# Kernel optimization log

Hardware: AMD Instinct MI355X
Metric: run time of the kernel (lower is better)

## Reference

```python
import jax, jax.numpy as jnp
import numpy as np

H = W = 32
C = 384
NH = 12
HEAD = C // NH
SCALE = HEAD ** -0.5
WS = 8            # window size
SS = 4            # shift size
N = WS * WS       # tokens per window (64)
NW = (H // WS) * (W // WS)  # windows per image (16)
HIDDEN = 4 * C
EPS = 1e-5
SQRT_2_OVER_PI = float(np.sqrt(2.0 / np.pi))


def _relative_position_index():
    ch = np.arange(WS)
    coords = np.stack(np.meshgrid(ch, ch, indexing='ij')).reshape(2, -1)  # [2, N]
    rel = (coords[:, :, None] - coords[:, None, :]).transpose(1, 2, 0)    # [N, N, 2]
    rel[:, :, 0] += WS - 1
    rel[:, :, 1] += WS - 1
    rel[:, :, 0] *= 2 * WS - 1
    return rel.sum(-1)  # [N, N] int


def _attn_mask():
    img = np.zeros((H, W), np.float32)
    sl = (slice(0, -WS), slice(-WS, -SS), slice(-SS, None))
    cnt = 0
    for hs in sl:
        for ws_ in sl:
            img[hs, ws_] = cnt
            cnt += 1
    m = img.reshape(H // WS, WS, W // WS, WS).transpose(0, 2, 1, 3).reshape(-1, N)  # [nW, N]
    am = m[:, None, :] - m[:, :, None]
    return np.where(am != 0, -100.0, 0.0).astype(np.float32)  # [nW, N, N]


REL_IDX = jnp.asarray(_relative_position_index())
ATTN_MASK = jnp.asarray(_attn_mask())


def _gelu(x):
    return x * 0.5 * (1.0 + jnp.tanh(SQRT_2_OVER_PI * (x + 0.044715 * x ** 3)))


def _layernorm(x, g, b):
    mu = jnp.mean(x, axis=-1, keepdims=True)
    var = jnp.mean(jnp.square(x - mu), axis=-1, keepdims=True)
    return (x - mu) * jax.lax.rsqrt(var + EPS) * g + b


def _window_partition(x):  # [B,H,W,C] -> [B*nW, N, C]
    B = x.shape[0]
    x = x.reshape(B, H // WS, WS, W // WS, WS, C).transpose(0, 1, 3, 2, 4, 5)
    return x.reshape(-1, N, C)


def _window_reverse(w, B):  # [B*nW, N, C] -> [B,H,W,C]
    x = w.reshape(B, H // WS, W // WS, WS, WS, C).transpose(0, 1, 3, 2, 4, 5)
    return x.reshape(B, H, W, C)


def setup_inputs() -> dict:
    key = jax.random.key(0)
    ks = jax.random.split(key, 16)
    s = 0.02
    return {
        'x': jax.random.normal(ks[0], (32, H * W, C), jnp.float32),
        'norm1_g': jnp.ones((C,), jnp.float32),
        'norm1_b': jnp.zeros((C,), jnp.float32),
        'qkv_w': jax.random.normal(ks[1], (C, 3 * C), jnp.float32) * s,
        'qkv_b': jnp.zeros((3 * C,), jnp.float32),
        'rel_bias_table': jax.random.normal(ks[2], ((2 * WS - 1) ** 2, NH), jnp.float32) * s,
        'proj_w': jax.random.normal(ks[3], (C, C), jnp.float32) * s,
        'proj_b': jnp.zeros((C,), jnp.float32),
        'norm2_g': jnp.ones((C,), jnp.float32),
        'norm2_b': jnp.zeros((C,), jnp.float32),
        'fc1_w': jax.random.normal(ks[4], (C, HIDDEN), jnp.float32) * s,
        'fc1_b': jnp.zeros((HIDDEN,), jnp.float32),
        'fc2_w': jax.random.normal(ks[5], (HIDDEN, C), jnp.float32) * s,
        'fc2_b': jnp.zeros((C,), jnp.float32),
    }


def reference(x, norm1_g, norm1_b, qkv_w, qkv_b, rel_bias_table, proj_w, proj_b,
              norm2_g, norm2_b, fc1_w, fc1_b, fc2_w, fc2_b):
    B = x.shape[0]
    shortcut = x
    y = _layernorm(x, norm1_g, norm1_b).reshape(B, H, W, C)
    y = jnp.roll(y, shift=(-SS, -SS), axis=(1, 2))          # cyclic shift
    win = _window_partition(y)                               # [B*nW, N, C]

    qkv = (win @ qkv_w + qkv_b).reshape(-1, N, 3, NH, HEAD).transpose(2, 0, 3, 1, 4)
    q, k, v = qkv[0], qkv[1], qkv[2]                         # [B*nW, NH, N, HEAD]
    attn = jnp.einsum('whnd,whmd->whnm', q * SCALE, k)       # [B*nW, NH, N, N]

    bias = rel_bias_table[REL_IDX.reshape(-1)].reshape(N, N, NH).transpose(2, 0, 1)
    attn = attn + bias[None]
    attn = attn.reshape(B, NW, NH, N, N) + ATTN_MASK[None, :, None]
    attn = jax.nn.softmax(attn.reshape(-1, NH, N, N), axis=-1)

    out = jnp.einsum('whnm,whmd->wnhd', attn, v).reshape(-1, N, C)
    out = out @ proj_w + proj_b                              # [B*nW, N, C]

    y = _window_reverse(out, B)
    y = jnp.roll(y, shift=(SS, SS), axis=(1, 2)).reshape(B, H * W, C)

    x = shortcut + y                                         # drop_path is identity (eval)
    h = _layernorm(x, norm2_g, norm2_b)
    h = _gelu(h @ fc1_w + fc1_b) @ fc2_w + fc2_b
    return x + h
```

## Files before the change

kernel.cpp:

```cpp
#include <hip/hip_runtime.h>
#include <hip/hip_bf16.h>
#include <math.h>

typedef __hip_bfloat16 bf16;
typedef __attribute__((ext_vector_type(8))) short short8;
typedef __attribute__((ext_vector_type(4))) float floatx4;

static constexpr int TOK = 32768;
static constexpr int CDIM = 384;
static constexpr int HID = 1536;

__device__ __forceinline__ bf16 f2bf(float v) { return __float2bfloat16(v); }

__device__ __forceinline__ unsigned short bf_bits(float a) {
  bf16 h = __float2bfloat16(a);
  unsigned short u;
  __builtin_memcpy(&u, &h, 2);
  return u;
}
__device__ __forceinline__ unsigned pack2(float a, float b) {
  return (unsigned)bf_bits(a) | ((unsigned)bf_bits(b) << 16);
}

typedef const __attribute__((address_space(1))) unsigned gas_t;
typedef __attribute__((address_space(3))) unsigned las_t;
__device__ __forceinline__ void gload16(const bf16* g, const bf16* l) {
  __builtin_amdgcn_global_load_lds((gas_t*)g, (las_t*)l, 16, 0, 0);
}

__global__ void k_convt(const float* __restrict__ src, bf16* __restrict__ dst,
                        int Kd, int Nd) {
  int tid = blockIdx.x * 256 + threadIdx.x;
  if (tid >= Kd * Nd) return;
  int k = tid / Nd, n = tid - k * Nd;
  dst[(size_t)n * Kd + k] = f2bf(src[tid]);
}

__global__ __launch_bounds__(256) void k_ln1(const float* __restrict__ x,
                                             const float* __restrict__ g,
                                             const float* __restrict__ b,
                                             bf16* __restrict__ out) {
  int wt = blockIdx.x * 4 + (threadIdx.x >> 6);
  int lane = threadIdx.x & 63;
  int win = wt >> 6, ntok = wt & 63;
  int bimg = win >> 4, wi = win & 15;
  int sh = (((wi >> 2) << 3) + (ntok >> 3) + 4) & 31;
  int sw = (((wi & 3) << 3) + (ntok & 7) + 4) & 31;
  const float* xr = x + ((size_t)bimg * 1024 + sh * 32 + sw) * CDIM;
  float v[6]; float s = 0.f, ss = 0.f;
#pragma unroll
  for (int j = 0; j < 6; ++j) {
    float t = xr[j * 64 + lane];
    v[j] = t; s += t; ss += t * t;
  }
#pragma unroll
  for (int off = 32; off > 0; off >>= 1) {
    s += __shfl_xor(s, off, 64);
    ss += __shfl_xor(ss, off, 64);
  }
  float mu = s * (1.f / 384.f);
  float var = ss * (1.f / 384.f) - mu * mu;
  float rs = rsqrtf(var + 1e-5f);
  bf16* orow = out + (size_t)wt * CDIM;
#pragma unroll
  for (int j = 0; j < 6; ++j) {
    int c = j * 64 + lane;
    orow[c] = f2bf((v[j] - mu) * rs * g[c] + b[c]);
  }
}

__global__ __launch_bounds__(256) void k_ln2(const float* __restrict__ x1,
                                             const float* __restrict__ g,
                                             const float* __restrict__ b,
                                             bf16* __restrict__ out) {
  int t = blockIdx.x * 4 + (threadIdx.x >> 6);
  int lane = threadIdx.x & 63;
  const float* xr = x1 + (size_t)t * CDIM;
  float v[6]; float s = 0.f, ss = 0.f;
#pragma unroll
  for (int j = 0; j < 6; ++j) {
    float q = xr[j * 64 + lane];
    v[j] = q; s += q; ss += q * q;
  }
#pragma unroll
  for (int off = 32; off > 0; off >>= 1) {
    s += __shfl_xor(s, off, 64);
    ss += __shfl_xor(ss, off, 64);
  }
  float mu = s * (1.f / 384.f);
  float var = ss * (1.f / 384.f) - mu * mu;
  float rs = rsqrtf(var + 1e-5f);
  bf16* orow = out + (size_t)t * CDIM;
#pragma unroll
  for (int j = 0; j < 6; ++j) {
    int c = j * 64 + lane;
    orow[c] = f2bf((v[j] - mu) * rs * g[c] + b[c]);
  }
}

template <int K, int EPI, int NT>
__global__ __launch_bounds__(256) void k_gemm(const bf16* __restrict__ A,
                                              const bf16* __restrict__ Bt,
                                              const float* __restrict__ bias,
                                              const float* __restrict__ extra,
                                              void* __restrict__ outp) {
  __shared__ __attribute__((aligned(16))) char pool[32768];
  bf16* As = (bf16*)pool;
  bf16* Bs = (bf16*)(pool + 16384);

  const int tid = threadIdx.x;
  const int wv = tid >> 6, lane = tid & 63;

  const int flat = blockIdx.x;
  const int xcd = flat & 7;
  const int idx = flat >> 3;
  const int rpx = (gridDim.x >> 3) / NT;
  const int cb = idx % NT;
  const int rb = idx / NT;
  const int mblk = (xcd * rpx + rb) * 128, nblk = cb * 128;

  const int srow = lane >> 3;
  const int scol8 = (lane & 7) ^ srow;
  const bf16* gaw = A + (size_t)(mblk + wv * 32 + srow) * K + scol8 * 8;
  const bf16* gbw = Bt + (size_t)(nblk + wv * 32 + srow) * K + scol8 * 8;
  const bf16* lAw = As + wv * 2048;
  const bf16* lBw = Bs + wv * 2048;

  const int wr = wv >> 1, wc = wv & 1;
  const int mr = lane & 15, q = lane >> 4;
  const bf16* faRow = As + (wr * 64 + mr) * 64;
  const bf16* fbRow = Bs + (wc * 64 + mr) * 64;
  const int sw0 = (q ^ (mr & 7)) * 8;
  const int sw4 = ((q + 4) ^ (mr & 7)) * 8;

  floatx4 acc[4][4];
#pragma unroll
  for (int i = 0; i < 4; ++i)
#pragma unroll
    for (int j = 0; j < 4; ++j) acc[i][j] = floatx4{0.f, 0.f, 0.f, 0.f};

  for (int k0 = 0; k0 < K; k0 += 64) {
    __syncthreads();
#pragma unroll
    for (int c = 0; c < 4; ++c) gload16(gaw + k0 + c * 8 * K, lAw + c * 512);
#pragma unroll
    for (int c = 0; c < 4; ++c) gload16(gbw + k0 + c * 8 * K, lBw + c * 512);
    __syncthreads();
    {
      short8 a[4], b[4];
#pragma unroll
      for (int mt = 0; mt < 4; ++mt) a[mt] = *(const short8*)(faRow + mt * 1024 + sw0);
#pragma unroll
      for (int nt = 0; nt < 4; ++nt) b[nt] = *(const short8*)(fbRow + nt * 1024 + sw0);
#pragma unroll
      for (int mt = 0; mt < 4; ++mt)
#pragma unroll
        for (int nt = 0; nt < 4; ++nt)
          acc[mt][nt] = __builtin_amdgcn_mfma_f32_16x16x32_bf16(a[mt], b[nt], acc[mt][nt], 0, 0, 0);
    }
    {
      short8 a[4], b[4];
#pragma unroll
      for (int mt = 0; mt < 4; ++mt) a[mt] = *(const short8*)(faRow + mt * 1024 + sw4);
#pragma unroll
      for (int nt = 0; nt < 4; ++nt) b[nt] = *(const short8*)(fbRow + nt * 1024 + sw4);
#pragma unroll
      for (int mt = 0; mt < 4; ++mt)
#pragma unroll
        for (int nt = 0; nt < 4; ++nt)
          acc[mt][nt] = __builtin_amdgcn_mfma_f32_16x16x32_bf16(a[mt], b[nt], acc[mt][nt], 0, 0, 0);
    }
  }

  __syncthreads();
  float* epsw = (float*)pool + wv * (16 * 68);
  const int rr = lane >> 2, c0 = (lane & 3) * 16;
#pragma unroll
  for (int mt = 0; mt < 4; ++mt) {
#pragma unroll
    for (int nt = 0; nt < 4; ++nt)
#pragma unroll
      for (int r = 0; r < 4; ++r)
        epsw[(q * 4 + r) * 68 + nt * 16 + mr] = acc[mt][nt][r];
    float v[16];
#pragma unroll
    for (int j = 0; j < 4; ++j) {
      float4 t = *(const float4*)&epsw[rr * 68 + c0 + j * 4];
      v[j * 4 + 0] = t.x; v[j * 4 + 1] = t.y; v[j * 4 + 2] = t.z; v[j * 4 + 3] = t.w;
    }
    const int grow = mblk + wr * 64 + mt * 16 + rr;
    const int gcol = nblk + wc * 64 + c0;

    if constexpr (EPI == 0) {
      int win = grow >> 6, ntok = grow & 63;
      int s = gcol / 384;
      int rem = gcol - s * 384;
      int h = rem >> 5, d0 = rem & 31;
      bf16* op = (bf16*)outp + (((size_t)s * 512 + win) * 12 + h) * 2048 + ntok * 32 + d0;
      uint4 pk;
      float bv[16];
#pragma unroll
      for (int j = 0; j < 16; ++j) bv[j] = v[j] + bias[gcol + j];
      pk.x = pack2(bv[0], bv[1]); pk.y = pack2(bv[2], bv[3]);
      pk.z = pack2(bv[4], bv[5]); pk.w = pack2(bv[6], bv[7]);
      *(uint4*)op = pk;
      pk.x = pack2(bv[8], bv[9]); pk.y = pack2(bv[10], bv[11]);
      pk.z = pack2(bv[12], bv[13]); pk.w = pack2(bv[14], bv[15]);
      *(uint4*)(op + 8) = pk;
    } else if constexpr (EPI == 1) {
      int win = grow >> 6, ntok = grow & 63;
      int bimg = win >> 4, wi = win & 15;
      int hh = (((wi >> 2) << 3) + (ntok >> 3) + 4) & 31;
      int ww = (((wi & 3) << 3) + (ntok & 7) + 4) & 31;
      size_t t = (size_t)bimg * 1024 + hh * 32 + ww;
      float* op = (float*)outp + t * CDIM + gcol;
      const float* xr = extra + t * CDIM + gcol;
#pragma unroll
      for (int j = 0; j < 4; ++j) {
        float4 xv = *(const float4*)(xr + j * 4);
        float4 ov;
        ov.x = xv.x + v[j * 4 + 0] + bias[gcol + j * 4 + 0];
        ov.y = xv.y + v[j * 4 + 1] + bias[gcol + j * 4 + 1];
        ov.z = xv.z + v[j * 4 + 2] + bias[gcol + j * 4 + 2];
        ov.w = xv.w + v[j * 4 + 3] + bias[gcol + j * 4 + 3];
        *(float4*)(op + j * 4) = ov;
      }
    } else if constexpr (EPI == 2) {
      float gv[16];
#pragma unroll
      for (int j = 0; j < 16; ++j) {
        float z = v[j] + bias[gcol + j];
        float u = 0.7978845608028654f * (z + 0.044715f * z * z * z);
        gv[j] = z / (1.f + __expf(-2.f * u));
      }
      bf16* op = (bf16*)outp + (size_t)grow * HID + gcol;
      uint4 pk;
      pk.x = pack2(gv[0], gv[1]); pk.y = pack2(gv[2], gv[3]);
      pk.z = pack2(gv[4], gv[5]); pk.w = pack2(gv[6], gv[7]);
      *(uint4*)op = pk;
      pk.x = pack2(gv[8], gv[9]); pk.y = pack2(gv[10], gv[11]);
      pk.z = pack2(gv[12], gv[13]); pk.w = pack2(gv[14], gv[15]);
      *(uint4*)(op + 8) = pk;
    } else {
      float* op = (float*)outp + (size_t)grow * CDIM + gcol;
      const float* xr = extra + (size_t)grow * CDIM + gcol;
#pragma unroll
      for (int j = 0; j < 4; ++j) {
        float4 xv = *(const float4*)(xr + j * 4);
        float4 ov;
        ov.x = xv.x + v[j * 4 + 0] + bias[gcol + j * 4 + 0];
        ov.y = xv.y + v[j * 4 + 1] + bias[gcol + j * 4 + 1];
        ov.z = xv.z + v[j * 4 + 2] + bias[gcol + j * 4 + 2];
        ov.w = xv.w + v[j * 4 + 3] + bias[gcol + j * 4 + 3];
        *(float4*)(op + j * 4) = ov;
      }
    }
  }
}

__global__ __launch_bounds__(64) void k_attn(const bf16* __restrict__ qkv,
                                             const float* __restrict__ tblg,
                                             bf16* __restrict__ out) {
  __shared__ __attribute__((aligned(16))) char pool[16384];
  bf16* Qs = (bf16*)pool;
  bf16* Ks = (bf16*)(pool + 5120);
  bf16* Ps = (bf16*)pool;
  float* Os = (float*)pool;
  bf16* Vt = (bf16*)(pool + 10240);
  unsigned long long* msk = (unsigned long long*)(pool + 14848);
  float* tbl = (float*)(pool + 15360);

  const int bid = blockIdx.x;
  const int win = bid / 12, head = bid - win * 12;
  const int lane = threadIdx.x;
  const int q = lane >> 4, mr = lane & 15;

  for (int i = lane; i < 225; i += 64) tbl[i] = tblg[i * 12 + head];

  size_t base = ((size_t)win * 12 + head) * 2048 + lane * 32;
  const uint4* qp = (const uint4*)(qkv + base);
  const uint4* kp = (const uint4*)(qkv + (size_t)12582912 + base);
  const uint4* vp = (const uint4*)(qkv + (size_t)25165824 + base);
#pragma unroll
  for (int i = 0; i < 4; ++i) *(uint4*)(Qs + lane * 40 + i * 8) = qp[i];
#pragma unroll
  for (int i = 0; i < 4; ++i) *(uint4*)(Ks + lane * 40 + i * 8) = kp[i];
  {
    union { uint4 u[4]; unsigned short h[32]; } vv;
#pragma unroll
    for (int i = 0; i < 4; ++i) vv.u[i] = vp[i];
    unsigned short* VtU = (unsigned short*)Vt;
#pragma unroll
    for (int d = 0; d < 32; ++d) VtU[d * 72 + lane] = vv.h[d];
  }
  {
    int wi = win & 15;
    int ri = lane >> 3, ci = lane & 7;
    int rh = ((wi >> 2) << 3) + ri, rw = ((wi & 3) << 3) + ci;
    int rid = (rh < 24 ? 0 : (rh < 28 ? 1 : 2)) * 3 + (rw < 24 ? 0 : (rw < 28 ? 1 : 2));
    unsigned long long m = 0;
#pragma unroll
    for (int v = 0; v < 9; ++v) {
      unsigned long long bb = __ballot(rid == v);
      if (rid == v) m = bb;
    }
    msk[lane] = m;
  }

  floatx4 sac[4][4];
#pragma unroll
  for (int i = 0; i < 4; ++i)
#pragma unroll
    for (int j = 0; j < 4; ++j) sac[i][j] = floatx4{0.f, 0.f, 0.f, 0.f};
  {
    short8 af[4], bf[4];
#pragma unroll
    for (int t = 0; t < 4; ++t) af[t] = *(const short8*)(Qs + (t * 16 + mr) * 40 + q * 8);
#pragma unroll
    for (int t = 0; t < 4; ++t) bf[t] = *(const short8*)(Ks + (t * 16 + mr) * 40 + q * 8);
#pragma unroll
    for (int mt = 0; mt < 4; ++mt)
#pragma unroll
      for (int nt = 0; nt < 4; ++nt)
        sac[mt][nt] = __builtin_amdgcn_mfma_f32_16x16x32_bf16(af[mt], bf[nt], sac[mt][nt], 0, 0, 0);
  }

  float psum[4][4];
#pragma unroll
  for (int mt = 0; mt < 4; ++mt)
#pragma unroll
    for (int r = 0; r < 4; ++r) psum[mt][r] = 0.f;
#pragma unroll
  for (int mt = 0; mt < 4; ++mt) {
#pragma unroll
    for (int r = 0; r < 4; ++r) {
      const int i = mt * 16 + q * 4 + r;
      const unsigned long long mrow = msk[i];
      const int bi = (i >> 3) * 15 + (i & 7);
#pragma unroll
      for (int nt = 0; nt < 4; ++nt) {
        const int j = nt * 16 + mr;
        const int idx = bi + 112 - (j >> 3) * 15 - (j & 7);
        float val = sac[mt][nt][r] * 0.17677669529663687f + tbl[idx];
        float p = __expf(val);
        p = ((mrow >> j) & 1ull) ? p : 0.f;
        psum[mt][r] += p;
        Ps[i * 72 + j] = f2bf(p);
      }
    }
  }
  float inv[4][4];
#pragma unroll
  for (int mt = 0; mt < 4; ++mt)
#pragma unroll
    for (int r = 0; r < 4; ++r) {
      float s = psum[mt][r];
      s += __shfl_xor(s, 1, 64);
      s += __shfl_xor(s, 2, 64);
      s += __shfl_xor(s, 4, 64);
      s += __shfl_xor(s, 8, 64);
      inv[mt][r] = 1.f / s;
    }

  floatx4 oac[4][2];
#pragma unroll
  for (int i = 0; i < 4; ++i)
#pragma unroll
    for (int j = 0; j < 2; ++j) oac[i][j] = floatx4{0.f, 0.f, 0.f, 0.f};
#pragma unroll
  for (int kk = 0; kk < 2; ++kk) {
    short8 ap[4], bv[2];
#pragma unroll
    for (int mt = 0; mt < 4; ++mt)
      ap[mt] = *(const short8*)(Ps + (mt * 16 + mr) * 72 + kk * 32 + q * 8);
#pragma unroll
    for (int nt = 0; nt < 2; ++nt)
      bv[nt] = *(const short8*)(Vt + (nt * 16 + mr) * 72 + kk * 32 + q * 8);
#pragma unroll
    for (int mt = 0; mt < 4; ++mt)
#pragma unroll
      for (int nt = 0; nt < 2; ++nt)
        oac[mt][nt] = __builtin_amdgcn_mfma_f32_16x16x32_bf16(ap[mt], bv[nt], oac[mt][nt], 0, 0, 0);
  }

#pragma unroll
  for (int mt = 0; mt < 4; ++mt)
#pragma unroll
    for (int nt = 0; nt < 2; ++nt)
#pragma unroll
      for (int r = 0; r < 4; ++r)
        Os[(mt * 16 + q * 4 + r) * 40 + nt * 16 + mr] = oac[mt][nt][r] * inv[mt][r];
  float ov[32];
#pragma unroll
  for (int c = 0; c < 8; ++c) {
    const int cc = c ^ (lane & 7);
    float4 t = *(const float4*)(Os + lane * 40 + cc * 4);
    ov[cc * 4 + 0] = t.x; ov[cc * 4 + 1] = t.y;
    ov[cc * 4 + 2] = t.z; ov[cc * 4 + 3] = t.w;
  }
  uint4* o4 = (uint4*)(out + ((size_t)win * 64 + lane) * CDIM + head * 32);
#pragma unroll
  for (int i = 0; i < 4; ++i) {
    uint4 pk;
    pk.x = pack2(ov[i * 8 + 0], ov[i * 8 + 1]);
    pk.y = pack2(ov[i * 8 + 2], ov[i * 8 + 3]);
    pk.z = pack2(ov[i * 8 + 4], ov[i * 8 + 5]);
    pk.w = pack2(ov[i * 8 + 6], ov[i * 8 + 7]);
    o4[i] = pk;
  }
}

extern "C" void kernel_launch(void* const* d_in, const int* in_sizes, int n_in,
                              void* d_out, int out_size, void* d_ws, size_t ws_size,
                              hipStream_t stream) {
  const float* x = (const float*)d_in[0];
  const float* n1g = (const float*)d_in[1];
  const float* n1b = (const float*)d_in[2];
  const float* qkv_w = (const float*)d_in[3];
  const float* qkv_b = (const float*)d_in[4];
  const float* reltbl = (const float*)d_in[5];
  const float* proj_w = (const float*)d_in[6];
  const float* proj_b = (const float*)d_in[7];
  const float* n2g = (const float*)d_in[8];
  const float* n2b = (const float*)d_in[9];
  const float* fc1_w = (const float*)d_in[10];
  const float* fc1_b = (const float*)d_in[11];
  const float* fc2_w = (const float*)d_in[12];
  const float* fc2_b = (const float*)d_in[13];
  float* out = (float*)d_out;

  char* p = (char*)d_ws;
  bf16* w_qkv_t = (bf16*)p;  p += (size_t)442368 * 2;
  bf16* w_proj_t = (bf16*)p; p += (size_t)147456 * 2;
  bf16* w_fc1_t = (bf16*)p;  p += (size_t)589824 * 2;
  bf16* w_fc2_t = (bf16*)p;  p += (size_t)589824 * 2;
  bf16* bufA = (bf16*)p;     p += (size_t)12582912 * 2;
  bf16* qkvb = (bf16*)p;     p += (size_t)37748736 * 2;
  bf16* attno = (bf16*)p;    p += (size_t)12582912 * 2;
  float* x1 = (float*)p;     p += (size_t)12582912 * 4;
  bf16* hidden = qkvb;

  k_convt<<<dim3((442368 + 255) / 256), dim3(256), 0, stream>>>(qkv_w, w_qkv_t, 384, 1152);
  k_convt<<<dim3((147456 + 255) / 256), dim3(256), 0, stream>>>(proj_w, w_proj_t, 384, 384);
  k_convt<<<dim3((589824 + 255) / 256), dim3(256), 0, stream>>>(fc1_w, w_fc1_t, 384, 1536);
  k_convt<<<dim3((589824 + 255) / 256), dim3(256), 0, stream>>>(fc2_w, w_fc2_t, 1536, 384);

  k_ln1<<<dim3(8192), dim3(256), 0, stream>>>(x, n1g, n1b, bufA);
  k_gemm<384, 0, 9><<<dim3(9 * 256), dim3(256), 0, stream>>>(bufA, w_qkv_t, qkv_b, nullptr, qkvb);
  k_attn<<<dim3(6144), dim3(64), 0, stream>>>(qkvb, reltbl, attno);
  k_gemm<384, 1, 3><<<dim3(3 * 256), dim3(256), 0, stream>>>(attno, w_proj_t, proj_b, x, x1);
  k_ln2<<<dim3(8192), dim3(256), 0, stream>>>(x1, n2g, n2b, bufA);
  k_gemm<384, 2, 12><<<dim3(12 * 256), dim3(256), 0, stream>>>(bufA, w_fc1_t, fc1_b, nullptr, hidden);
  k_gemm<1536, 3, 3><<<dim3(3 * 256), dim3(256), 0, stream>>>(hidden, w_fc2_t, fc2_b, x1, out);
}
```

Before: 435.8 us.

## Register-prefetch GEMM tiles and use narrower N tiles for N=384 GEMMs

Replaces the direct global-to-LDS loads with register-staged prefetch: the next K slice is loaded into registers while MFMAs run on the current LDS tile, then written to LDS at the top of the next iteration. It also adds a TN template parameter so the proj and fc2 GEMMs (N=384) use 128x64 tiles. This doubles their grid from 768 to 1536 blocks for better CU occupancy, at the cost of less reuse of A. The register staging raises VGPR use and loses the async LDS-load path.

```diff
diff --git a/kernel.cpp b/kernel.cpp
--- a/kernel.cpp
+++ b/kernel.cpp
@@ -20,12 +20,6 @@
 }
 __device__ __forceinline__ unsigned pack2(float a, float b) {
   return (unsigned)bf_bits(a) | ((unsigned)bf_bits(b) << 16);
-}
-
-typedef const __attribute__((address_space(1))) unsigned gas_t;
-typedef __attribute__((address_space(3))) unsigned las_t;
-__device__ __forceinline__ void gload16(const bf16* g, const bf16* l) {
-  __builtin_amdgcn_global_load_lds((gas_t*)g, (las_t*)l, 16, 0, 0);
 }
 
 __global__ void k_convt(const float* __restrict__ src, bf16* __restrict__ dst,
@@ -98,13 +92,15 @@
   }
 }
 
-template <int K, int EPI, int NT>
+template <int K, int EPI, int NT, int TN>
 __global__ __launch_bounds__(256) void k_gemm(const bf16* __restrict__ A,
                                               const bf16* __restrict__ Bt,
                                               const float* __restrict__ bias,
                                               const float* __restrict__ extra,
                                               void* __restrict__ outp) {
-  __shared__ __attribute__((aligned(16))) char pool[32768];
+  constexpr int NB = (TN == 128) ? 4 : 2;
+  constexpr int MT = (TN == 128) ? 4 : 2;
+  __shared__ __attribute__((aligned(16))) char pool[16384 + NB * 4096];
   bf16* As = (bf16*)pool;
   bf16* Bs = (bf16*)(pool + 16384);
 
@@ -117,55 +113,68 @@
   const int rpx = (gridDim.x >> 3) / NT;
   const int cb = idx % NT;
   const int rb = idx / NT;
-  const int mblk = (xcd * rpx + rb) * 128, nblk = cb * 128;
+  const int mblk = (xcd * rpx + rb) * 128, nblk = cb * TN;
 
   const int srow = lane >> 3;
   const int scol8 = (lane & 7) ^ srow;
   const bf16* gaw = A + (size_t)(mblk + wv * 32 + srow) * K + scol8 * 8;
-  const bf16* gbw = Bt + (size_t)(nblk + wv * 32 + srow) * K + scol8 * 8;
-  const bf16* lAw = As + wv * 2048;
-  const bf16* lBw = Bs + wv * 2048;
-
-  const int wr = wv >> 1, wc = wv & 1;
+  const bf16* gbw = Bt + (size_t)(nblk + wv * (NB * 8) + srow) * K + scol8 * 8;
+
+  const int wrow = (TN == 128) ? (wv >> 1) * 64 : wv * 32;
+  const int wcol = (TN == 128) ? (wv & 1) * 64 : 0;
   const int mr = lane & 15, q = lane >> 4;
-  const bf16* faRow = As + (wr * 64 + mr) * 64;
-  const bf16* fbRow = Bs + (wc * 64 + mr) * 64;
+  const bf16* faRow = As + (wrow + mr) * 64;
+  const bf16* fbRow = Bs + (wcol + mr) * 64;
   const int sw0 = (q ^ (mr & 7)) * 8;
   const int sw4 = ((q + 4) ^ (mr & 7)) * 8;
 
-  floatx4 acc[4][4];
-#pragma unroll
-  for (int i = 0; i < 4; ++i)
+  floatx4 acc[MT][4];
+#pragma unroll
+  for (int i = 0; i < MT; ++i)
 #pragma unroll
     for (int j = 0; j < 4; ++j) acc[i][j] = floatx4{0.f, 0.f, 0.f, 0.f};
+
+  uint4 ra[4], rb_[NB];
+#pragma unroll
+  for (int c = 0; c < 4; ++c) ra[c] = *(const uint4*)(gaw + c * 8 * K);
+#pragma unroll
+  for (int c = 0; c < NB; ++c) rb_[c] = *(const uint4*)(gbw + c * 8 * K);
 
   for (int k0 = 0; k0 < K; k0 += 64) {
     __syncthreads();
 #pragma unroll
-    for (int c = 0; c < 4; ++c) gload16(gaw + k0 + c * 8 * K, lAw + c * 512);
-#pragma unroll
-    for (int c = 0; c < 4; ++c) gload16(gbw + k0 + c * 8 * K, lBw + c * 512);
+    for (int c = 0; c < 4; ++c)
+      *(uint4*)(As + wv * 2048 + c * 512 + lane * 8) = ra[c];
+#pragma unroll
+    for (int c = 0; c < NB; ++c)
+      *(uint4*)(Bs + wv * (NB * 512) + c * 512 + lane * 8) = rb_[c];
     __syncthreads();
+    if (k0 + 64 < K) {
+#pragma unroll
+      for (int c = 0; c < 4; ++c) ra[c] = *(const uint4*)(gaw + k0 + 64 + c * 8 * K);
+#pragma unroll
+      for (int c = 0; c < NB; ++c) rb_[c] = *(const uint4*)(gbw + k0 + 64 + c * 8 * K);
+    }
     {
-      short8 a[4], b[4];
-#pragma unroll
-      for (int mt = 0; mt < 4; ++mt) a[mt] = *(const short8*)(faRow + mt * 1024 + sw0);
+      short8 a[MT], b[4];
+#pragma unroll
+      for (int mt = 0; mt < MT; ++mt) a[mt] = *(const short8*)(faRow + mt * 1024 + sw0);
 #pragma unroll
       for (int nt = 0; nt < 4; ++nt) b[nt] = *(const short8*)(fbRow + nt * 1024 + sw0);
 #pragma unroll
-      for (int mt = 0; mt < 4; ++mt)
+      for (int mt = 0; mt < MT; ++mt)
 #pragma unroll
         for (int nt = 0; nt < 4; ++nt)
           acc[mt][nt] = __builtin_amdgcn_mfma_f32_16x16x32_bf16(a[mt], b[nt], acc[mt][nt], 0, 0, 0);
     }
     {
-      short8 a[4], b[4];
-#pragma unroll
-      for (int mt = 0; mt < 4; ++mt) a[mt] = *(const short8*)(faRow + mt * 1024 + sw4);
+      short8 a[MT], b[4];
+#pragma unroll
+      for (int mt = 0; mt < MT; ++mt) a[mt] = *(const short8*)(faRow + mt * 1024 + sw4);
 #pragma unroll
       for (int nt = 0; nt < 4; ++nt) b[nt] = *(const short8*)(fbRow + nt * 1024 + sw4);
 #pragma unroll
-      for (int mt = 0; mt < 4; ++mt)
+      for (int mt = 0; mt < MT; ++mt)
 #pragma unroll
         for (int nt = 0; nt < 4; ++nt)
           acc[mt][nt] = __builtin_amdgcn_mfma_f32_16x16x32_bf16(a[mt], b[nt], acc[mt][nt], 0, 0, 0);
@@ -176,7 +185,7 @@
   float* epsw = (float*)pool + wv * (16 * 68);
   const int rr = lane >> 2, c0 = (lane & 3) * 16;
 #pragma unroll
-  for (int mt = 0; mt < 4; ++mt) {
+  for (int mt = 0; mt < MT; ++mt) {
 #pragma unroll
     for (int nt = 0; nt < 4; ++nt)
 #pragma unroll
@@ -188,8 +197,8 @@
       float4 t = *(const float4*)&epsw[rr * 68 + c0 + j * 4];
       v[j * 4 + 0] = t.x; v[j * 4 + 1] = t.y; v[j * 4 + 2] = t.z; v[j * 4 + 3] = t.w;
     }
-    const int grow = mblk + wr * 64 + mt * 16 + rr;
-    const int gcol = nblk + wc * 64 + c0;
+    const int grow = mblk + wrow + mt * 16 + rr;
+    const int gcol = nblk + wcol + c0;
 
     if constexpr (EPI == 0) {
       int win = grow >> 6, ntok = grow & 63;
@@ -446,10 +455,10 @@
   k_convt<<<dim3((589824 + 255) / 256), dim3(256), 0, stream>>>(fc2_w, w_fc2_t, 1536, 384);
 
   k_ln1<<<dim3(8192), dim3(256), 0, stream>>>(x, n1g, n1b, bufA);
-  k_gemm<384, 0, 9><<<dim3(9 * 256), dim3(256), 0, stream>>>(bufA, w_qkv_t, qkv_b, nullptr, qkvb);
+  k_gemm<384, 0, 9, 128><<<dim3(9 * 256), dim3(256), 0, stream>>>(bufA, w_qkv_t, qkv_b, nullptr, qkvb);
   k_attn<<<dim3(6144), dim3(64), 0, stream>>>(qkvb, reltbl, attno);
-  k_gemm<384, 1, 3><<<dim3(3 * 256), dim3(256), 0, stream>>>(attno, w_proj_t, proj_b, x, x1);
+  k_gemm<384, 1, 6, 64><<<dim3(6 * 256), dim3(256), 0, stream>>>(attno, w_proj_t, proj_b, x, x1);
   k_ln2<<<dim3(8192), dim3(256), 0, stream>>>(x1, n2g, n2b, bufA);
-  k_gemm<384, 2, 12><<<dim3(12 * 256), dim3(256), 0, stream>>>(bufA, w_fc1_t, fc1_b, nullptr, hidden);
-  k_gemm<1536, 3, 3><<<dim3(3 * 256), dim3(256), 0, stream>>>(hidden, w_fc2_t, fc2_b, x1, out);
-}
+  k_gemm<384, 2, 12, 128><<<dim3(12 * 256), dim3(256), 0, stream>>>(bufA, w_fc1_t, fc1_b, nullptr, hidden);
+  k_gemm<1536, 3, 6, 64><<<dim3(6 * 256), dim3(256), 0, stream>>>(hidden, w_fc2_t, fc2_b, x1, out);
+}
```

After: 946.1 us. 117% more time.
